# Kernel optimization log

Measured on AMD Instinct MI355X. Metric: run time of the kernel, lower is better.

The kernel has to match this reference:

```python
import jax, jax.numpy as jnp
import numpy as np


def _lstm_cell(x, h, c, Wih, Whh, b):
    # torch gate order: input, forget, cell(g), output
    gates = x @ Wih.T + h @ Whh.T + b  # [B, 4H]
    i, f, g, o = jnp.split(gates, 4, axis=-1)
    i = jax.nn.sigmoid(i)
    f = jax.nn.sigmoid(f)
    g = jnp.tanh(g)
    o = jax.nn.sigmoid(o)
    c = f * c + i * g
    return o * jnp.tanh(c), c


def setup_inputs() -> dict:
    key = jax.random.key(0)
    ks = jax.random.split(key, 20)
    B, Te, Td, X, H = 4096, 168, 24, 8, 64
    s = 0.1  # weight scale for numerical sanity in the AR sampling loop
    return {
        "enc_x": jax.random.normal(ks[0], (B, Te, X), jnp.float32),
        "enc_z": jax.random.uniform(ks[1], (B, Te, 1), jnp.float32),
        "dec_x": jax.random.normal(ks[2], (B, Td, X - 1), jnp.float32),
        "v": jax.random.uniform(ks[3], (B, 1, 1), jnp.float32) + 0.5,  # positive scale
        "eps": jax.random.normal(ks[4], (B, Td, 1), jnp.float32),
        "W_ih0": s * jax.random.normal(ks[5], (4 * H, X), jnp.float32),
        "W_hh0": s * jax.random.normal(ks[6], (4 * H, H), jnp.float32),
        "b0": s * jax.random.normal(ks[7], (4 * H,), jnp.float32),
        "W_ih1": s * jax.random.normal(ks[8], (4 * H, H), jnp.float32),
        "W_hh1": s * jax.random.normal(ks[9], (4 * H, H), jnp.float32),
        "b1": s * jax.random.normal(ks[10], (4 * H,), jnp.float32),
        "W_ih2": s * jax.random.normal(ks[11], (4 * H, H), jnp.float32),
        "W_hh2": s * jax.random.normal(ks[12], (4 * H, H), jnp.float32),
        "b2": s * jax.random.normal(ks[13], (4 * H,), jnp.float32),
        "w_m": s * jax.random.normal(ks[14], (H, 1), jnp.float32),
        "b_m": jnp.zeros((1,), jnp.float32),
        "w_a": s * jax.random.normal(ks[15], (H, 1), jnp.float32),
        "b_a": jnp.zeros((1,), jnp.float32),
    }


def reference(enc_x, enc_z, dec_x, v, eps,
              W_ih0, W_hh0, b0, W_ih1, W_hh1, b1, W_ih2, W_hh2, b2,
              w_m, b_m, w_a, b_a):
    B = enc_x.shape[0]
    H = W_hh0.shape[1]

    def step3(x, h, c):
        h0, c0 = _lstm_cell(x, h[0], c[0], W_ih0, W_hh0, b0)
        h1, c1 = _lstm_cell(h0, h[1], c[1], W_ih1, W_hh1, b1)
        h2, c2 = _lstm_cell(h1, h[2], c[2], W_ih2, W_hh2, b2)
        return (h0, h1, h2), (c0, c1, c2), h2

    z0 = jnp.zeros((B, H), enc_x.dtype)
    h = (z0, z0, z0)
    c = (z0, z0, z0)

    # ---- encoder: 3-layer LSTM over Te steps ----
    def enc_step(carry, x_t):
        h, c = carry
        h, c, _ = step3(x_t, h, c)
        return (h, c), None

    (h, c), _ = jax.lax.scan(enc_step, (h, c), jnp.swapaxes(enc_x, 0, 1))

    vf = v[:, 0, :]                 # [B, 1]
    z = enc_z[:, -1, :] / vf        # [B, 1]

    def dec_step(carry, inp):
        h, c, z = carry
        x_t, e_t = inp              # [B, X-1], [B, 1]
        x = jnp.concatenate([z, x_t], axis=-1)   # [B, X]
        h, c, o = step3(x, h, c)
        m = (o @ w_m + b_m) * vf                  # Gaussian mean, rescaled
        a = jax.nn.softplus(o @ w_a + b_a) * vf   # Gaussian std, rescaled
        zs = m + a * e_t                          # reparameterized sample
        return (h, c, zs / vf), zs

    xs = (jnp.swapaxes(dec_x, 0, 1), jnp.swapaxes(eps, 0, 1))
    _, Z = jax.lax.scan(dec_step, (h, c, z), xs)  # [Td, B, 1]
    return jnp.swapaxes(Z, 0, 1)                  # [B, Td, 1]
```

## Files before the change

kernel.cpp:

```cpp
#include <hip/hip_runtime.h>
#include <math.h>

#define B_TOT 4096
#define TE 168
#define TD 24
#define NWG 256
#define HSTR 72

typedef _Float16 f16;
typedef __attribute__((ext_vector_type(8))) _Float16 f16x8;
typedef __attribute__((ext_vector_type(4))) float f32x4;

#define SCL_S (-1.4426950408889634f)
#define SCL_G (2.885390081777927f)

__global__ __launch_bounds__(256) void pack_kernel(
    const float* __restrict__ Wih0, const float* __restrict__ Whh0,
    const float* __restrict__ Wih1, const float* __restrict__ Whh1,
    const float* __restrict__ Wih2, const float* __restrict__ Whh2,
    f16* __restrict__ pk)
{
    int idx = blockIdx.x * 256 + threadIdx.x;
    int j = idx & 7;
    int t = idx >> 3;
    int ln = t & 63; t >>= 6;
    int c  = t & 3;  t >>= 2;
    int q  = t & 3;  t >>= 2;
    int l  = t % 3;
    int w  = t / 3;
    int row = q * 64 + w * 16 + (ln & 15);
    int k   = c * 32 + ((ln >> 4) << 3) + j;
    float val = 0.f;
    if (l == 0) {
        if (k < 8)                 val = Wih0[row * 8 + k];
        else if (k >= 32 && k < 96) val = Whh0[row * 64 + (k - 32)];
    } else if (l == 1) {
        val = (k < 64) ? Wih1[row * 64 + k] : Whh1[row * 64 + (k - 64)];
    } else {
        val = (k < 64) ? Wih2[row * 64 + k] : Whh2[row * 64 + (k - 64)];
    }
    const float sc = (q == 2) ? SCL_G : SCL_S;
    pk[idx] = (f16)(val * sc);
}

__device__ __forceinline__ float softplusf(float x) {
    float t = fabsf(x) * 1.4426950408889634f;
    float E = __builtin_amdgcn_exp2f(-t);
    float L = __builtin_amdgcn_logf(1.f + E);
    return fmaxf(x, 0.f) + 0.6931471805599453f * L;
}

__global__ __launch_bounds__(768, 3) void lstm_kernel(
    const float* __restrict__ enc_x, const float* __restrict__ enc_z,
    const float* __restrict__ dec_x, const float* __restrict__ v,
    const float* __restrict__ eps,   const f16* __restrict__ pk,
    const float* __restrict__ b0, const float* __restrict__ b1,
    const float* __restrict__ b2,
    const float* __restrict__ w_m, const float* __restrict__ b_m,
    const float* __restrict__ w_a, const float* __restrict__ b_a,
    float* __restrict__ out)
{
    const int tid  = threadIdx.x;
    const int lane = tid & 63;
    const int wv   = (tid >> 6) & 3;
    const int role = tid >> 8;
    const int bg   = blockIdx.x * 16;
    const int m16  = lane & 15;
    const int quad = lane >> 4;

    __shared__ f16   hbuf[2][3][16][HSTR];
    __shared__ float zbuf[16];

    {
        uint* hz = (uint*)&hbuf[0][0][0][0];
        const int HW = 2 * 3 * 16 * HSTR / 2;
        for (int i = tid; i < HW; i += 768) hz[i] = 0u;
    }

    f16x8 wgt[4][4];
#define PKOFF(l, q, c) ((((((size_t)wv * 3 + (l)) * 4 + (q)) * 4 + (c)) * 64 + lane) * 8)
    {
        const f16* pkr = pk + PKOFF(role, 0, 0);
#pragma unroll
        for (int q = 0; q < 4; ++q)
#pragma unroll
            for (int c = 0; c < 4; ++c)
                wgt[c][q] = *(const f16x8*)(pkr + (q * 4 + c) * 64 * 8);
    }
#undef PKOFF

    const int hid_self = wv * 16 + m16;
    f32x4 bsp[4];
    {
        const float* bp = (role == 0) ? b0 : (role == 1) ? b1 : b2;
#pragma unroll
        for (int q = 0; q < 4; ++q) {
            const float sc = (q == 2) ? SCL_G : SCL_S;
            float bv = bp[q * 64 + hid_self] * sc;
            bsp[q] = (f32x4){bv, bv, bv, bv};
        }
    }

    f16* hb = &hbuf[0][0][0][0];
    const int aoff = m16 * HSTR + quad * 8;
    float cst[4] = {};

#define RBAR                                                                  \
    {                                                                         \
        asm volatile("s_waitcnt lgkmcnt(0)" ::: "memory");                    \
        __builtin_amdgcn_s_barrier();                                         \
        asm volatile("" ::: "memory");                                        \
    }

#define PRIO_UP __builtin_amdgcn_s_setprio(1)
#define PRIO_DN __builtin_amdgcn_s_setprio(0)

#define HBASE(pp, l) (hb + ((pp) * 3 + (l)) * (16 * HSTR))
#define MFMA16(af, bf, cf) __builtin_amdgcn_mfma_f32_16x16x32_f16(af, bf, cf, 0, 0, 0)

#define MM_R(P, areg, wi)                                                     \
    {                                                                         \
        P##0 = MFMA16(areg, wgt[wi][0], bsp[0]);                              \
        P##1 = MFMA16(areg, wgt[wi][1], bsp[1]);                              \
        P##2 = MFMA16(areg, wgt[wi][2], bsp[2]);                              \
        P##3 = MFMA16(areg, wgt[wi][3], bsp[3]);                              \
    }
#define MM_F(P, aptr, wi)                                                     \
    {                                                                         \
        f16x8 af = *(const f16x8*)(aptr);                                     \
        P##0 = MFMA16(af, wgt[wi][0], bsp[0]);                                \
        P##1 = MFMA16(af, wgt[wi][1], bsp[1]);                                \
        P##2 = MFMA16(af, wgt[wi][2], bsp[2]);                                \
        P##3 = MFMA16(af, wgt[wi][3], bsp[3]);                                \
    }
#define MM(P, aptr, wi)                                                       \
    {                                                                         \
        f16x8 af = *(const f16x8*)(aptr);                                     \
        P##0 = MFMA16(af, wgt[wi][0], P##0);                                  \
        P##1 = MFMA16(af, wgt[wi][1], P##1);                                  \
        P##2 = MFMA16(af, wgt[wi][2], P##2);                                  \
        P##3 = MFMA16(af, wgt[wi][3], P##3);                                  \
    }

#define CELL(P, lh, PP)                                                       \
    {                                                                         \
        f16* hw = HBASE(PP, lh) + hid_self;                                   \
        _Pragma("unroll")                                                     \
        for (int r = 0; r < 4; ++r) {                                         \
            float Ei = __builtin_amdgcn_exp2f(P##0[r]);                       \
            float Ef = __builtin_amdgcn_exp2f(P##1[r]);                       \
            float Eg = __builtin_amdgcn_exp2f(P##2[r]);                       \
            float Eo = __builtin_amdgcn_exp2f(P##3[r]);                       \
            float ef1 = 1.f + Ef;                                             \
            float pig = (1.f + Ei) * (1.f + Eg);                              \
            float R   = __builtin_amdgcn_rcpf(pig * ef1);                     \
            float fv  = pig * R;                                              \
            float ig  = (Eg - 1.f) * ef1 * R;                                 \
            float cn  = fmaf(fv, cst[r], ig);                                 \
            cst[r] = cn;                                                      \
            float Ec  = __builtin_amdgcn_exp2f(cn * SCL_G);                   \
            float Roc = __builtin_amdgcn_rcpf((1.f + Eo) * (1.f + Ec));       \
            hw[(quad * 4 + r) * HSTR] = (f16)((Ec - 1.f) * Roc);              \
        }                                                                     \
    }

    const float* xp = enc_x + (size_t)(bg + m16) * (TE * 8);
    f32x4 xa = {}, xb = {};
    f16x8 af_cur = {};
    if (role == 0) {
        xa = *(const f32x4*)xp; xb = *(const f32x4*)(xp + 4);
#pragma unroll
        for (int j = 0; j < 4; ++j) { af_cur[j] = (f16)xa[j]; af_cur[4 + j] = (f16)xb[j]; }
    }

#define ROUND(PP, D0, D1, D2, T0)                                             \
    {                                                                         \
        RBAR;                                                                 \
        f32x4 a0, a1, a2, a3;                                                 \
        if (role == 0) {                                                      \
            if (D0) {                                                         \
                PRIO_UP;                                                      \
                MM_R(a, af_cur, 0);                                           \
                const f16* h0p = HBASE(1 - (PP), 0) + aoff;                   \
                MM(a, h0p, 1);                                                \
                MM(a, h0p + 32, 2);                                           \
                PRIO_DN;                                                      \
                if ((T0) + 1 < TE) {                                          \
                    xa = *(const f32x4*)(xp + (size_t)((T0) + 1) * 8);        \
                    xb = *(const f32x4*)(xp + (size_t)((T0) + 1) * 8 + 4);    \
                }                                                             \
                CELL(a, 0, PP);                                               \
                if ((T0) + 1 < TE) {                                          \
                    _Pragma("unroll")                                         \
                    for (int j = 0; j < 4; ++j) {                             \
                        af_cur[j] = (f16)xa[j]; af_cur[4 + j] = (f16)xb[j];   \
                    }                                                         \
                }                                                             \
            }                                                                 \
        } else if (role == 1) {                                               \
            if (D1) {                                                         \
                PRIO_UP;                                                      \
                const f16* h0p = HBASE(1 - (PP), 0) + aoff;                   \
                const f16* h1p = HBASE(1 - (PP), 1) + aoff;                   \
                MM_F(a, h0p, 0);                                              \
                MM(a, h0p + 32, 1);                                           \
                MM(a, h1p, 2);                                                \
                MM(a, h1p + 32, 3);                                           \
                PRIO_DN;                                                      \
                CELL(a, 1, PP);                                               \
            }                                                                 \
        } else {                                                              \
            if (D2) {                                                         \
                PRIO_UP;                                                      \
                const f16* h1p = HBASE(1 - (PP), 1) + aoff;                   \
                const f16* h2p = HBASE(1 - (PP), 2) + aoff;                   \
                MM_F(a, h1p, 0);                                              \
                MM(a, h1p + 32, 1);                                           \
                MM(a, h2p, 2);                                                \
                MM(a, h2p + 32, 3);                                           \
                PRIO_DN;                                                      \
                CELL(a, 2, PP);                                               \
            }                                                                 \
        }                                                                     \
    }

    ROUND(0, 1, 0, 0, 0)
    ROUND(1, 1, 1, 0, 1)
    for (int t = 2; t < 166; t += 2) {
        ROUND(0, 1, 1, 1, t)
        ROUND(1, 1, 1, 1, t + 1)
    }
    ROUND(0, 1, 1, 1, 166)
    ROUND(1, 1, 1, 1, 167)
    ROUND(0, 0, 1, 1, 168)
    ROUND(1, 0, 0, 1, 169)

    const int   mH = (tid >> 4) & 15;
    const float vf = (role == 0) ? v[bg + mH] : 0.f;
    float wmr[4], war[4];
#pragma unroll
    for (int r = 0; r < 4; ++r) {
        wmr[r] = w_m[(tid & 15) + 16 * r];
        war[r] = w_a[(tid & 15) + 16 * r];
    }
    const float bmv = b_m[0], bav = b_a[0];
    if (role == 0 && (tid & 15) == 0)
        zbuf[mH] = enc_z[(size_t)(bg + mH) * TE + (TE - 1)] / vf;

    float dxr[7];
    if (role == 0) {
#pragma unroll
        for (int j = 0; j < 7; ++j)
            dxr[j] = dec_x[((size_t)(bg + m16) * TD + 0) * 7 + j];
    }

    for (int t = 0; t < TD; ++t) {
        const int PA = t & 1;
        float ev = 0.f;
        RBAR;
        {
            f32x4 a0, a1, a2, a3;
            if (role == 0) {
                float zq = zbuf[m16];
                ev = eps[(size_t)(bg + mH) * TD + t];
                f16x8 af;
                af[0] = (f16)zq;
#pragma unroll
                for (int j = 0; j < 7; ++j) af[1 + j] = (f16)dxr[j];
                if (t + 1 < TD) {
#pragma unroll
                    for (int j = 0; j < 7; ++j)
                        dxr[j] = dec_x[((size_t)(bg + m16) * TD + (t + 1)) * 7 + j];
                }
                MM_R(a, af, 0);
                const f16* h0p = HBASE(1 - PA, 0) + aoff;
                MM(a, h0p, 1);
                MM(a, h0p + 32, 2);
                CELL(a, 0, PA);
            }
        }
        RBAR;
        {
            f32x4 a0, a1, a2, a3;
            if (role == 1) {
                const f16* h0p = HBASE(PA, 0) + aoff;
                const f16* h1p = HBASE(PA, 1) + aoff;
                MM_F(a, h0p, 0);
                MM(a, h0p + 32, 1);
                MM(a, h1p, 2);
                MM(a, h1p + 32, 3);
                CELL(a, 1, 1 - PA);
            }
        }
        RBAR;
        {
            f32x4 a0, a1, a2, a3;
            if (role == 2) {
                const f16* h1p = HBASE(1 - PA, 1) + aoff;
                const f16* h2p = HBASE(1 - PA, 2) + aoff;
                MM_F(a, h1p, 0);
                MM(a, h1p + 32, 1);
                MM(a, h2p, 2);
                MM(a, h2p + 32, 3);
                CELL(a, 2, PA);
            }
        }
        RBAR;
        if (role == 0) {
            float sm = 0.f, sa = 0.f;
            const f16* h2p = HBASE(PA, 2) + mH * HSTR;
#pragma unroll
            for (int r = 0; r < 4; ++r) {
                float hv = (float)h2p[(tid & 15) + 16 * r];
                sm += hv * wmr[r];
                sa += hv * war[r];
            }
#pragma unroll
            for (int off = 1; off < 16; off <<= 1) {
                sm += __shfl_xor(sm, off, 64);
                sa += __shfl_xor(sa, off, 64);
            }
            if ((tid & 15) == 0) {
                float mo  = (sm + bmv) * vf;
                float ao  = softplusf(sa + bav) * vf;
                float zsv = mo + ao * ev;
                out[(size_t)(bg + mH) * TD + t] = zsv;
                zbuf[mH] = zsv / vf;
            }
        }
    }

#undef RBAR
#undef PRIO_UP
#undef PRIO_DN
#undef HBASE
#undef MFMA16
#undef MM_R
#undef MM_F
#undef MM
#undef CELL
#undef ROUND
}

extern "C" void kernel_launch(void* const* d_in, const int* in_sizes, int n_in,
                              void* d_out, int out_size, void* d_ws, size_t ws_size,
                              hipStream_t stream) {
    const float* enc_x = (const float*)d_in[0];
    const float* enc_z = (const float*)d_in[1];
    const float* dec_x = (const float*)d_in[2];
    const float* v     = (const float*)d_in[3];
    const float* eps   = (const float*)d_in[4];
    const float* Wih0  = (const float*)d_in[5];
    const float* Whh0  = (const float*)d_in[6];
    const float* b0    = (const float*)d_in[7];
    const float* Wih1  = (const float*)d_in[8];
    const float* Whh1  = (const float*)d_in[9];
    const float* b1    = (const float*)d_in[10];
    const float* Wih2  = (const float*)d_in[11];
    const float* Whh2  = (const float*)d_in[12];
    const float* b2    = (const float*)d_in[13];
    const float* w_m   = (const float*)d_in[14];
    const float* b_m   = (const float*)d_in[15];
    const float* w_a   = (const float*)d_in[16];
    const float* b_a   = (const float*)d_in[17];
    float* out = (float*)d_out;
    f16*   pk  = (f16*)d_ws;

    pack_kernel<<<384, 256, 0, stream>>>(Wih0, Whh0, Wih1, Whh1, Wih2, Whh2, pk);
    lstm_kernel<<<NWG, 768, 0, stream>>>(enc_x, enc_z, dec_x, v, eps, pk,
                                         b0, b1, b2, w_m, b_m, w_a, b_a, out);
}
```

Measured before the change: 308.0 us.

## Restructure decoder loop to overlap head and layer-0 precompute with other layers

Rewrites the autoregressive decoder loop so layer 0 precomputes its dec_x and recurrent contributions one step ahead while layer 1 runs. The z-dependent input column is then added as a rank-1 FMA correction, using the fp32 first-column weights of W_ih0, once the head result is ready. The output head is recomputed redundantly per lane with vector loads and a two-stage shuffle reduction, which removes the zbuf shared round trip and one barrier per step. Layers 1 and 2 prefetch their recurrent h operands before the barrier. Only the 24-step decoder is affected, so any effect on total time is limited, and the extra precompute adds register pressure.

```diff
diff --git a/kernel.cpp b/kernel.cpp
--- a/kernel.cpp
+++ b/kernel.cpp
@@ -54,6 +54,7 @@
     const float* __restrict__ enc_x, const float* __restrict__ enc_z,
     const float* __restrict__ dec_x, const float* __restrict__ v,
     const float* __restrict__ eps,   const f16* __restrict__ pk,
+    const float* __restrict__ Wih0,
     const float* __restrict__ b0, const float* __restrict__ b1,
     const float* __restrict__ b2,
     const float* __restrict__ w_m, const float* __restrict__ b_m,
@@ -68,8 +69,7 @@
     const int m16  = lane & 15;
     const int quad = lane >> 4;
 
-    __shared__ f16   hbuf[2][3][16][HSTR];
-    __shared__ float zbuf[16];
+    __shared__ f16 hbuf[2][3][16][HSTR];
 
     {
         uint* hz = (uint*)&hbuf[0][0][0][0];
@@ -124,6 +124,13 @@
         P##1 = MFMA16(areg, wgt[wi][1], bsp[1]);                              \
         P##2 = MFMA16(areg, wgt[wi][2], bsp[2]);                              \
         P##3 = MFMA16(areg, wgt[wi][3], bsp[3]);                              \
+    }
+#define MM_RACC(P, areg, wi)                                                  \
+    {                                                                         \
+        P##0 = MFMA16(areg, wgt[wi][0], P##0);                                \
+        P##1 = MFMA16(areg, wgt[wi][1], P##1);                                \
+        P##2 = MFMA16(areg, wgt[wi][2], P##2);                                \
+        P##3 = MFMA16(areg, wgt[wi][3], P##3);                                \
     }
 #define MM_F(P, aptr, wi)                                                     \
     {                                                                         \
@@ -235,100 +242,128 @@
     ROUND(0, 0, 1, 1, 168)
     ROUND(1, 0, 0, 1, 169)
 
-    const int   mH = (tid >> 4) & 15;
-    const float vf = (role == 0) ? v[bg + mH] : 0.f;
-    float wmr[4], war[4];
-#pragma unroll
-    for (int r = 0; r < 4; ++r) {
-        wmr[r] = w_m[(tid & 15) + 16 * r];
-        war[r] = w_a[(tid & 15) + 16 * r];
-    }
-    const float bmv = b_m[0], bav = b_a[0];
-    if (role == 0 && (tid & 15) == 0)
-        zbuf[mH] = enc_z[(size_t)(bg + mH) * TE + (TE - 1)] / vf;
-
-    float dxr[7];
+    float vf = 0.f, rvf = 0.f, bmv = 0.f, bav = 0.f, zn = 0.f, ep_cur = 0.f;
+    float dxr[7] = {};
+    float w0[4]  = {};
+    f32x4 wmv4[4] = {}, wav4[4] = {};
     if (role == 0) {
+        vf  = v[bg + m16];
+        rvf = 1.0f / vf;
+        bmv = b_m[0]; bav = b_a[0];
+        zn  = enc_z[(size_t)(bg + m16) * TE + (TE - 1)] / vf;
 #pragma unroll
         for (int j = 0; j < 7; ++j)
             dxr[j] = dec_x[((size_t)(bg + m16) * TD + 0) * 7 + j];
+#pragma unroll
+        for (int q = 0; q < 4; ++q)
+            w0[q] = Wih0[(q * 64 + hid_self) * 8] * ((q == 2) ? SCL_G : SCL_S);
+#pragma unroll
+        for (int i = 0; i < 4; ++i) {
+            wmv4[i] = *(const f32x4*)(w_m + quad * 16 + 4 * i);
+            wav4[i] = *(const f32x4*)(w_a + quad * 16 + 4 * i);
+        }
+    }
+
+    f32x4 a0, a1, a2, a3;
+    f16x8 pr_a = {}, pr_b = {};
+
+#define HEAD(tOut, ppRead)                                                    \
+    {                                                                         \
+        const f16* h2p = HBASE(ppRead, 2) + m16 * HSTR + quad * 16;           \
+        f16x8 ha = *(const f16x8*)h2p;                                        \
+        f16x8 hc = *(const f16x8*)(h2p + 8);                                  \
+        float sm = 0.f, sa = 0.f;                                             \
+        _Pragma("unroll")                                                     \
+        for (int i = 0; i < 4; ++i) {                                         \
+            _Pragma("unroll")                                                 \
+            for (int j = 0; j < 4; ++j) {                                     \
+                float hv = (i < 2) ? (float)ha[i * 4 + j]                     \
+                                   : (float)hc[(i - 2) * 4 + j];              \
+                sm = fmaf(hv, wmv4[i][j], sm);                                \
+                sa = fmaf(hv, wav4[i][j], sa);                                \
+            }                                                                 \
+        }                                                                     \
+        sm += __shfl_xor(sm, 16, 64); sm += __shfl_xor(sm, 32, 64);           \
+        sa += __shfl_xor(sa, 16, 64); sa += __shfl_xor(sa, 32, 64);           \
+        float mo = (sm + bmv) * vf;                                           \
+        float ao = softplusf(sa + bav) * vf;                                  \
+        float zs = fmaf(ao, ep_cur, mo);                                      \
+        if (tid < 16) out[(size_t)(bg + m16) * TD + (tOut)] = zs;             \
+        zn = zs * rvf;                                                        \
     }
 
     for (int t = 0; t < TD; ++t) {
         const int PA = t & 1;
-        float ev = 0.f;
-        RBAR;
-        {
-            f32x4 a0, a1, a2, a3;
-            if (role == 0) {
-                float zq = zbuf[m16];
-                ev = eps[(size_t)(bg + mH) * TD + t];
+        if (role == 0) {
+            if (t > 0) { HEAD(t - 1, 1 - PA); }
+            if (t == 0) {
                 f16x8 af;
-                af[0] = (f16)zq;
+                af[0] = (f16)zn;
 #pragma unroll
                 for (int j = 0; j < 7; ++j) af[1 + j] = (f16)dxr[j];
-                if (t + 1 < TD) {
-#pragma unroll
-                    for (int j = 0; j < 7; ++j)
-                        dxr[j] = dec_x[((size_t)(bg + m16) * TD + (t + 1)) * 7 + j];
-                }
                 MM_R(a, af, 0);
-                const f16* h0p = HBASE(1 - PA, 0) + aoff;
+                const f16* h0p = HBASE(1, 0) + aoff;
                 MM(a, h0p, 1);
                 MM(a, h0p + 32, 2);
-                CELL(a, 0, PA);
+            } else {
+#pragma unroll
+                for (int r = 0; r < 4; ++r) {
+                    float zr = __shfl(zn, (lane & 48) + quad * 4 + r, 64);
+                    a0[r] = fmaf(w0[0], zr, a0[r]);
+                    a1[r] = fmaf(w0[1], zr, a1[r]);
+                    a2[r] = fmaf(w0[2], zr, a2[r]);
+                    a3[r] = fmaf(w0[3], zr, a3[r]);
+                }
             }
+            CELL(a, 0, PA);
+            if (t + 1 < TD) {
+#pragma unroll
+                for (int j = 0; j < 7; ++j)
+                    dxr[j] = dec_x[((size_t)(bg + m16) * TD + (t + 1)) * 7 + j];
+            }
+            ep_cur = eps[(size_t)(bg + m16) * TD + t];
+        } else if (role == 1) {
+            const f16* h1p = HBASE(PA, 1) + aoff;
+            pr_a = *(const f16x8*)h1p;
+            pr_b = *(const f16x8*)(h1p + 32);
+        } else {
+            const f16* h2p = HBASE(1 - PA, 2) + aoff;
+            pr_a = *(const f16x8*)h2p;
+            pr_b = *(const f16x8*)(h2p + 32);
         }
         RBAR;
-        {
-            f32x4 a0, a1, a2, a3;
-            if (role == 1) {
-                const f16* h0p = HBASE(PA, 0) + aoff;
-                const f16* h1p = HBASE(PA, 1) + aoff;
-                MM_F(a, h0p, 0);
-                MM(a, h0p + 32, 1);
-                MM(a, h1p, 2);
-                MM(a, h1p + 32, 3);
-                CELL(a, 1, 1 - PA);
-            }
+
+        if (role == 1) {
+            const f16* h0p = HBASE(PA, 0) + aoff;
+            MM_F(a, h0p, 0);
+            MM(a, h0p + 32, 1);
+            MM_RACC(a, pr_a, 2);
+            MM_RACC(a, pr_b, 3);
+            CELL(a, 1, 1 - PA);
+        } else if (role == 0 && t + 1 < TD) {
+            f16x8 afx = {};
+            afx[0] = (f16)0.f;
+#pragma unroll
+            for (int j = 0; j < 7; ++j) afx[1 + j] = (f16)dxr[j];
+            MM_R(a, afx, 0);
+            const f16* h0p = HBASE(PA, 0) + aoff;
+            MM(a, h0p, 1);
+            MM(a, h0p + 32, 2);
         }
         RBAR;
-        {
-            f32x4 a0, a1, a2, a3;
-            if (role == 2) {
-                const f16* h1p = HBASE(1 - PA, 1) + aoff;
-                const f16* h2p = HBASE(1 - PA, 2) + aoff;
-                MM_F(a, h1p, 0);
-                MM(a, h1p + 32, 1);
-                MM(a, h2p, 2);
-                MM(a, h2p + 32, 3);
-                CELL(a, 2, PA);
-            }
+
+        if (role == 2) {
+            const f16* h1p = HBASE(1 - PA, 1) + aoff;
+            MM_F(a, h1p, 0);
+            MM(a, h1p + 32, 1);
+            MM_RACC(a, pr_a, 2);
+            MM_RACC(a, pr_b, 3);
+            CELL(a, 2, PA);
         }
         RBAR;
-        if (role == 0) {
-            float sm = 0.f, sa = 0.f;
-            const f16* h2p = HBASE(PA, 2) + mH * HSTR;
-#pragma unroll
-            for (int r = 0; r < 4; ++r) {
-                float hv = (float)h2p[(tid & 15) + 16 * r];
-                sm += hv * wmr[r];
-                sa += hv * war[r];
-            }
-#pragma unroll
-            for (int off = 1; off < 16; off <<= 1) {
-                sm += __shfl_xor(sm, off, 64);
-                sa += __shfl_xor(sa, off, 64);
-            }
-            if ((tid & 15) == 0) {
-                float mo  = (sm + bmv) * vf;
-                float ao  = softplusf(sa + bav) * vf;
-                float zsv = mo + ao * ev;
-                out[(size_t)(bg + mH) * TD + t] = zsv;
-                zbuf[mH] = zsv / vf;
-            }
-        }
-    }
+    }
+
+    if (role == 0) { HEAD(TD - 1, 1); }
 
 #undef RBAR
 #undef PRIO_UP
@@ -336,10 +371,12 @@
 #undef HBASE
 #undef MFMA16
 #undef MM_R
+#undef MM_RACC
 #undef MM_F
 #undef MM
 #undef CELL
 #undef ROUND
+#undef HEAD
 }
 
 extern "C" void kernel_launch(void* const* d_in, const int* in_sizes, int n_in,
@@ -367,6 +404,6 @@
     f16*   pk  = (f16*)d_ws;
 
     pack_kernel<<<384, 256, 0, stream>>>(Wih0, Whh0, Wih1, Whh1, Wih2, Whh2, pk);
-    lstm_kernel<<<NWG, 768, 0, stream>>>(enc_x, enc_z, dec_x, v, eps, pk,
+    lstm_kernel<<<NWG, 768, 0, stream>>>(enc_x, enc_z, dec_x, v, eps, pk, Wih0,
                                          b0, b1, b2, w_m, b_m, w_a, b_a, out);
 }
```

After: 368.7 us. 19.7% more time.
